# Kernel tuning notes

Hardware: AMD Instinct MI355X
Metric: run time of the kernel (lower is better)

Reference implementation:

```python
import jax, jax.numpy as jnp
import numpy as np

M, N, IN_DIM, NITER = 32, 32, 1024, 100
ALPHA, SIGMA = 0.3, 16.0  # sigma default = max(m, n) / 2
BATCH = 16384


def setup_inputs() -> dict:
    key = jax.random.key(0)
    k1, k2 = jax.random.split(key)
    x = jax.random.normal(k1, (BATCH, IN_DIM), dtype=jnp.float32)
    weights = jax.random.normal(k2, (IN_DIM, M * N), dtype=jnp.float32)
    ii, jj = jnp.meshgrid(jnp.arange(M), jnp.arange(N), indexing='ij')
    locations = jnp.stack([ii.ravel(), jj.ravel()], axis=1).astype(jnp.int32)  # (m*n, 2), row-major like the generator
    return {"x": x, "weights": weights, "locations": locations, "current_iter": 10}


def reference(x, weights, locations, current_iter):
    # x: (B, in_dim); weights: (in_dim, m*n); locations: (m*n, 2)
    B = x.shape[0]
    # Euclidean distances from each sample to each neuron, via ||a-b||^2 expansion
    x2 = jnp.sum(x * x, axis=1, keepdims=True)            # (B, 1)
    w2 = jnp.sum(weights * weights, axis=0)[None, :]      # (1, m*n)
    d2 = jnp.clip(x2 + w2 - 2.0 * (x @ weights), 0.0, None)
    dists = jnp.sqrt(d2)                                  # (B, m*n)
    loss_per = jnp.min(dists, axis=1)                     # (B,)
    bmu_index = jnp.argmin(dists, axis=1)                 # (B,)
    iter_correction = 1.0 - current_iter / NITER
    lr = ALPHA * iter_correction
    sigma = SIGMA * iter_correction
    loc_f = locations.astype(jnp.float32)                 # (m*n, 2)
    bmu_loc = loc_f[bmu_index]                            # (B, 2)
    # squared grid distance of every neuron to each sample's BMU
    dsq = jnp.sum((loc_f[None, :, :] - bmu_loc[:, None, :]) ** 2, axis=2)  # (B, m*n)
    lr_locations = jnp.exp(-dsq / (sigma * sigma)) * lr   # (B, m*n)
    # delta[i,k] = (1/B) * sum_b lr_locations[b,k] * (x[b,i] - weights[i,k])
    # computed without materializing the (B, in_dim, m*n) broadcast tensor
    pos = jnp.einsum('bk,bi->ik', lr_locations, x)        # (in_dim, m*n)
    neg = weights * jnp.sum(lr_locations, axis=0)[None, :]
    delta = (pos - neg) / B
    new_weights = weights + delta
    loss = jnp.sum(loss_per) / B
    return loss, new_weights
```

## Files before the change

### kernel.cpp

```cpp
#include <hip/hip_runtime.h>

typedef unsigned short u16;
typedef short bf16x8 __attribute__((ext_vector_type(8)));
typedef float f32x4 __attribute__((ext_vector_type(4)));

#define BATCH   16384
#define INDIM   1024
#define KNEUR   1024

__device__ __forceinline__ u16 f2bf(float f) {
  union { float f; unsigned u; } v; v.f = f;
  unsigned r = v.u + 0x7FFFu + ((v.u >> 16) & 1u);
  return (u16)(r >> 16);
}
__device__ __forceinline__ float bf2f(u16 h) {
  union { unsigned u; float f; } v; v.u = ((unsigned)h) << 16; return v.f;
}

#define GLDS(gp, lp) __builtin_amdgcn_global_load_lds( \
  (const __attribute__((address_space(1))) void*)(gp), \
  (__attribute__((address_space(3))) void*)(lp), 16, 0, 0)

#define RAWBAR() __builtin_amdgcn_s_barrier()
#define LGKM0() do { asm volatile("s_waitcnt lgkmcnt(0)" ::: "memory"); \
                     __builtin_amdgcn_sched_barrier(0); } while (0)
#define VMC6() asm volatile("s_waitcnt vmcnt(6)" ::: "memory")
#define VMC0() asm volatile("s_waitcnt vmcnt(0)" ::: "memory")

__global__ __launch_bounds__(256)
void k_prep(const float* __restrict__ x, u16* __restrict__ xb, float* __restrict__ x2,
            const float* __restrict__ w, u16* __restrict__ wt, float* __restrict__ w2,
            const int* __restrict__ loc, const int* __restrict__ itp,
            u16* __restrict__ Tb, float* __restrict__ Tf,
            float* __restrict__ Xf, int* __restrict__ cntcur, float* __restrict__ S) {
  __shared__ float tile[64][65];
  __shared__ float red[4][64];
  int bid = blockIdx.x;
  int t = threadIdx.x;
  if (bid < 4096) {
    int row = bid * 4 + (t >> 6);
    int l = t & 63;
    const float* xr = x + (size_t)row * INDIM;
    u16* xbr = xb + (size_t)row * INDIM;
    float s = 0.f;
    #pragma unroll
    for (int seg = 0; seg < 4; ++seg) {
      float4 v = *(const float4*)(xr + seg * 256 + l * 4);
      ushort4 o; o.x = f2bf(v.x); o.y = f2bf(v.y); o.z = f2bf(v.z); o.w = f2bf(v.w);
      *(ushort4*)(xbr + seg * 256 + l * 4) = o;
      s += v.x * v.x + v.y * v.y + v.z * v.z + v.w * v.w;
    }
    for (int m = 32; m; m >>= 1) s += __shfl_xor(s, m, 64);
    if (l == 0) x2[row] = s;
  } else if (bid < 8192) {
    int id = (bid - 4096) * 256 + t;
    int c = id >> 10, k = id & 1023;
    float corr = 1.f - (float)itp[0] / 100.f;
    float lr = 0.3f * corr;
    float sig = 16.f * corr;
    float inv_s2 = 1.f / (sig * sig);
    int di = loc[2 * c] - loc[2 * k];
    int dj = loc[2 * c + 1] - loc[2 * k + 1];
    float v = lr * __expf(-(float)(di * di + dj * dj) * inv_s2);
    Tf[id] = v;
    Tb[id] = f2bf(v);
    Xf[id] = 0.f;
    if (id < 2304) cntcur[id] = 0;
    if (id < 1024) S[id] = 0.f;
  } else if (bid < 8448) {
    int bb = bid - 8192;
    int bi = bb & 15;
    int bj = bb >> 4;
    int tx = t & 63, ty = t >> 6;
    int i0 = bj * 64, k0 = bi * 64;
    for (int r = ty; r < 64; r += 4)
      tile[r][tx] = w[(size_t)(i0 + r) * KNEUR + k0 + tx];
    __syncthreads();
    for (int r = ty; r < 64; r += 4)
      wt[(size_t)(k0 + r) * INDIM + i0 + tx] = f2bf(tile[tx][r]);
  } else {
    int tx = t & 63, ty = t >> 6;
    int k = (bid - 8448) * 64 + tx;
    float s = 0.f;
    for (int i = ty * 256; i < ty * 256 + 256; ++i) {
      float v = w[(size_t)i * KNEUR + k];
      s += v * v;
    }
    red[ty][tx] = s;
    __syncthreads();
    if (ty == 0) w2[k] = red[0][tx] + red[1][tx] + red[2][tx] + red[3][tx];
  }
}

__global__ __launch_bounds__(512, 2)
void k_gemm1_8p(const u16* __restrict__ A, const u16* __restrict__ Bm,
                const float* __restrict__ x2, const float* __restrict__ w2,
                float* __restrict__ pmin, int* __restrict__ pidx) {
  __shared__ __align__(16) u16 lds[2][2][2][128 * 64];
  __shared__ float s_rv[2][256];
  __shared__ int   s_ri[2][256];

  int bid = blockIdx.x;
  int swz = (bid & 7) * 32 + (bid >> 3);
  int mb = swz >> 2, nb = swz & 3;
  int tid = threadIdx.x;
  int lane = tid & 63;
  int wm = (tid >> 6) >> 1, wn = (tid >> 6) & 1;

  const size_t rowA0 = (size_t)mb * 256;
  const size_t rowB0 = (size_t)nb * 256;

  auto STAGE = [&](int u, int op, int qh) {
    if (u >= 16) return;
    const u16* src = (op == 0) ? (A + (rowA0 + qh * 128) * 1024)
                               : (Bm + (rowB0 + qh * 128) * 1024);
    int k0 = u * 64;
    u16* dst0 = &lds[u & 1][op][qh][0];
    #pragma unroll
    for (int j = 0; j < 2; ++j) {
      int s = j * 512 + tid;
      int r = s >> 3;
      int cs = (s & 7) ^ (r & 7);
      GLDS(src + (size_t)r * 1024 + k0 + cs * 8, dst0 + (size_t)s * 8);
    }
  };
  auto LDA = [&](bf16x8 (&a)[2][2], int db, int qm) {
    #pragma unroll
    for (int mt = 0; mt < 2; ++mt)
      #pragma unroll
      for (int kk = 0; kk < 2; ++kk) {
        int row = wm * 32 + mt * 16 + (lane & 15);
        int ch = (kk * 4 + (lane >> 4)) ^ (row & 7);
        a[mt][kk] = *(const bf16x8*)(&lds[db][0][qm][row * 64 + ch * 8]);
      }
  };
  auto LDB = [&](bf16x8 (&b)[4][2], int db, int qn) {
    #pragma unroll
    for (int nt = 0; nt < 4; ++nt)
      #pragma unroll
      for (int kk = 0; kk < 2; ++kk) {
        int row = wn * 64 + nt * 16 + (lane & 15);
        int ch = (kk * 4 + (lane >> 4)) ^ (row & 7);
        b[nt][kk] = *(const bf16x8*)(&lds[db][1][qn][row * 64 + ch * 8]);
      }
  };

  f32x4 acc[2][2][2][4];
  #pragma unroll
  for (int i = 0; i < 2; ++i)
    #pragma unroll
    for (int j = 0; j < 2; ++j)
      #pragma unroll
      for (int m = 0; m < 2; ++m)
        #pragma unroll
        for (int n = 0; n < 4; ++n) {
          acc[i][j][m][n][0] = 0.f; acc[i][j][m][n][1] = 0.f;
          acc[i][j][m][n][2] = 0.f; acc[i][j][m][n][3] = 0.f;
        }

  bf16x8 a[2][2], b0[4][2], b1[4][2];

  #define PHASE(accq, av, bv) do { \
    __builtin_amdgcn_s_setprio(1); \
    _Pragma("unroll") \
    for (int mt = 0; mt < 2; ++mt) \
      _Pragma("unroll") \
      for (int nt = 0; nt < 4; ++nt) \
        _Pragma("unroll") \
        for (int kk = 0; kk < 2; ++kk) \
          accq[mt][nt] = __builtin_amdgcn_mfma_f32_16x16x32_bf16(av[mt][kk], bv[nt][kk], accq[mt][nt], 0, 0, 0); \
    __builtin_amdgcn_s_setprio(0); \
  } while (0)

  STAGE(0, 0, 0); STAGE(0, 1, 1); STAGE(0, 0, 1); STAGE(0, 1, 0);
  STAGE(1, 0, 0); STAGE(1, 1, 1); STAGE(1, 0, 1);
  VMC6();
  RAWBAR();

  #pragma unroll 2
  for (int t = 0; t < 16; ++t) {
    int db = t & 1;
    LDA(a, db, 0); LDB(b0, db, 0);
    STAGE(t + 1, 1, 0);
    RAWBAR(); LGKM0();
    PHASE(acc[0][0], a, b0);
    RAWBAR();
    LDB(b1, db, 1);
    STAGE(t + 2, 0, 0);
    RAWBAR(); LGKM0();
    PHASE(acc[0][1], a, b1);
    RAWBAR();
    LDA(a, db, 1);
    STAGE(t + 2, 1, 1);
    RAWBAR(); LGKM0();
    PHASE(acc[1][1], a, b1);
    RAWBAR();
    STAGE(t + 2, 0, 1);
    RAWBAR(); LGKM0();
    PHASE(acc[1][0], a, b0);
    if (t < 14) { VMC6(); } else { VMC0(); }
    RAWBAR();
  }

  int g = lane >> 4, li = lane & 15;
  #pragma unroll
  for (int qm = 0; qm < 2; ++qm)
    #pragma unroll
    for (int mt = 0; mt < 2; ++mt)
      #pragma unroll
      for (int rr = 0; rr < 4; ++rr) {
        int lrow = qm * 128 + wm * 32 + mt * 16 + g * 4 + rr;
        float xv = x2[rowA0 + lrow];
        float v = 1e30f; int vi = 0x7fffffff;
        #pragma unroll
        for (int qn = 0; qn < 2; ++qn)
          #pragma unroll
          for (int nt = 0; nt < 4; ++nt) {
            int col = (int)rowB0 + qn * 128 + wn * 64 + nt * 16 + li;
            float d2 = xv + w2[col] - 2.f * acc[qm][qn][mt][nt][rr];
            if (d2 < v) { v = d2; vi = col; }
          }
        #pragma unroll
        for (int m = 1; m < 16; m <<= 1) {
          float ov = __shfl_xor(v, m, 64);
          int oi = __shfl_xor(vi, m, 64);
          if (ov < v || (ov == v && oi < vi)) { v = ov; vi = oi; }
        }
        if (li == 0) { s_rv[wn][lrow] = v; s_ri[wn][lrow] = vi; }
      }
  __syncthreads();
  if (tid < 256) {
    float v0 = s_rv[0][tid], v1 = s_rv[1][tid];
    int i0 = s_ri[0][tid], i1 = s_ri[1][tid];
    float v = v0; int vi = i0;
    if (v1 < v0 || (v1 == v0 && i1 < i0)) { v = v1; vi = i1; }
    size_t brow = rowA0 + tid;
    pmin[brow * 4 + nb] = v;
    pidx[brow * 4 + nb] = vi;
  }
  #undef PHASE
}

__global__ __launch_bounds__(256, 4)
void k_gemm2(const u16* __restrict__ A, const u16* __restrict__ Bm,
             float* __restrict__ outw) {
  __shared__ __align__(16) u16 ldsA[128 * 64];
  __shared__ __align__(16) u16 ldsB[128 * 64];

  int bid = blockIdx.x;
  int ks = bid & 3;
  int tile = bid >> 2;
  int mb = tile >> 3, nb = tile & 7;
  int ktlo = ks * 4, kthi = ktlo + 4;
  int lane = threadIdx.x & 63;
  int wid = threadIdx.x >> 6;
  int wr = wid >> 1, wc = wid & 1;

  f32x4 acc[4][4];
  #pragma unroll
  for (int i = 0; i < 4; ++i)
    #pragma unroll
    for (int j = 0; j < 4; ++j) { acc[i][j][0] = 0.f; acc[i][j][1] = 0.f; acc[i][j][2] = 0.f; acc[i][j][3] = 0.f; }

  const size_t rowA0 = (size_t)mb * 128;
  const size_t rowB0 = (size_t)nb * 128;

  for (int kt = ktlo; kt < kthi; ++kt) {
    int k0 = kt * 64;
    __syncthreads();
    #pragma unroll
    for (int q = 0; q < 4; ++q) {
      int p = q * 256 + wid * 64 + lane;
      int row = p >> 3;
      int clog = (p & 7) ^ (row & 7);
      GLDS(A + (rowA0 + row) * 1024 + k0 + clog * 8,
           ldsA + (size_t)(q * 256 + wid * 64) * 8);
    }
    #pragma unroll
    for (int q = 0; q < 4; ++q) {
      int p = q * 256 + wid * 64 + lane;
      int row = p >> 3;
      int clog = (p & 7) ^ (row & 7);
      GLDS(Bm + (rowB0 + row) * 1024 + k0 + clog * 8,
           ldsB + (size_t)(q * 256 + wid * 64) * 8);
    }
    __syncthreads();
    #pragma unroll
    for (int kk = 0; kk < 2; ++kk) {
      bf16x8 af[4], bfr[4];
      #pragma unroll
      for (int mt = 0; mt < 4; ++mt) {
        int row = wr * 64 + mt * 16 + (lane & 15);
        int ch = (kk * 4 + (lane >> 4)) ^ (row & 7);
        af[mt] = *(const bf16x8*)(ldsA + row * 64 + ch * 8);
      }
      #pragma unroll
      for (int nt = 0; nt < 4; ++nt) {
        int row = wc * 64 + nt * 16 + (lane & 15);
        int ch = (kk * 4 + (lane >> 4)) ^ (row & 7);
        bfr[nt] = *(const bf16x8*)(ldsB + row * 64 + ch * 8);
      }
      #pragma unroll
      for (int mt = 0; mt < 4; ++mt)
        #pragma unroll
        for (int nt = 0; nt < 4; ++nt)
          acc[mt][nt] = __builtin_amdgcn_mfma_f32_16x16x32_bf16(af[mt], bfr[nt], acc[mt][nt], 0, 0, 0);
    }
  }

  const float invB = 1.f / (float)BATCH;
  #pragma unroll
  for (int mt = 0; mt < 4; ++mt)
    #pragma unroll
    for (int nt = 0; nt < 4; ++nt)
      #pragma unroll
      for (int r = 0; r < 4; ++r) {
        int i = (int)rowA0 + wr * 64 + mt * 16 + (lane >> 4) * 4 + r;
        int k = (int)rowB0 + wc * 64 + nt * 16 + (lane & 15);
        atomicAdd(&outw[(size_t)i * KNEUR + k], acc[mt][nt][r] * invB);
      }
}

__global__ void k_bmu_scan(const float* __restrict__ pmin, const int* __restrict__ pidx,
                           int* __restrict__ bmu, float* __restrict__ lpart,
                           int* __restrict__ cnt, int* __restrict__ ticket,
                           int* __restrict__ cursor, float* __restrict__ cntf,
                           float* __restrict__ out) {
  int t = threadIdx.x;
  int b = blockIdx.x * 256 + t;
  float v = 1e30f; int vi = 0;
  #pragma unroll
  for (int j = 0; j < 4; ++j) {
    float pv = pmin[(size_t)b * 4 + j];
    if (pv < v) { v = pv; vi = pidx[(size_t)b * 4 + j]; }
  }
  bmu[b] = vi;
  atomicAdd(&cnt[vi], 1);
  float d = sqrtf(fmaxf(v, 0.f));
  __shared__ float red[256];
  red[t] = d;
  __syncthreads();
  for (int s = 128; s > 0; s >>= 1) {
    if (t < s) red[t] += red[t + s];
    __syncthreads();
  }
  if (t == 0) lpart[blockIdx.x] = red[0];

  __threadfence();
  __shared__ int is_last;
  if (t == 0) is_last = (atomicAdd(ticket, 1) == 63);
  __syncthreads();
  if (!is_last) return;

  __shared__ int sc[256];
  int4 c4 = *(const int4*)(cnt + 4 * t);
  int tsum = c4.x + c4.y + c4.z + c4.w;
  sc[t] = tsum;
  __syncthreads();
  for (int off = 1; off < 256; off <<= 1) {
    int val = sc[t];
    int add = (t >= off) ? sc[t - off] : 0;
    __syncthreads();
    sc[t] = val + add;
    __syncthreads();
  }
  int excl = sc[t] - tsum;
  cursor[4 * t + 0] = excl;
  cursor[4 * t + 1] = excl + c4.x;
  cursor[4 * t + 2] = excl + c4.x + c4.y;
  cursor[4 * t + 3] = excl + c4.x + c4.y + c4.z;
  cntf[4 * t + 0] = (float)c4.x;
  cntf[4 * t + 1] = (float)c4.y;
  cntf[4 * t + 2] = (float)c4.z;
  cntf[4 * t + 3] = (float)c4.w;
  if (t < 64) {
    float l = lpart[t];
    for (int m = 32; m; m >>= 1) l += __shfl_xor(l, m, 64);
    if (t == 0) out[0] = l * (1.f / (float)BATCH);
  }
}

__global__ void k_place_S(const int* __restrict__ bmu, int* __restrict__ cursor,
                          int* __restrict__ perm,
                          const float* __restrict__ cntf, const float* __restrict__ Tf,
                          float* __restrict__ S) {
  int bid = blockIdx.x;
  int t = threadIdx.x;
  if (bid < 64) {
    int b = bid * 256 + t;
    int c = bmu[b];
    int p = atomicAdd(&cursor[c], 1);
    perm[p] = b;
  } else {
    int chunk = bid - 64;
    int cchunk = chunk >> 2;
    int kb = chunk & 3;
    int k = kb * 256 + t;
    float s = 0.f;
    for (int c = cchunk * 64; c < cchunk * 64 + 64; ++c)
      s += cntf[c] * Tf[(size_t)c * KNEUR + k];
    atomicAdd(&S[k], s);
  }
}

__global__ __launch_bounds__(256)
void k_xsum2(const int* __restrict__ perm, const int* __restrict__ bmu,
             const u16* __restrict__ xb, float* __restrict__ Xf) {
  int t = threadIdx.x;
  int m0 = blockIdx.x * 32;
  int pm[32], cl[32];
  #pragma unroll
  for (int j = 0; j < 32; ++j) pm[j] = perm[m0 + j];
  #pragma unroll
  for (int j = 0; j < 32; ++j) cl[j] = bmu[pm[j]];
  float a0 = 0.f, a1 = 0.f, a2 = 0.f, a3 = 0.f;
  int ccur = cl[0];
  #pragma unroll
  for (int j = 0; j < 32; ++j) {
    if (cl[j] != ccur) {
      float* p = Xf + (size_t)ccur * INDIM + 4 * t;
      atomicAdd(p + 0, a0); atomicAdd(p + 1, a1);
      atomicAdd(p + 2, a2); atomicAdd(p + 3, a3);
      a0 = a1 = a2 = a3 = 0.f;
      ccur = cl[j];
    }
    ushort4 v = *(const ushort4*)(xb + (size_t)pm[j] * INDIM + t * 4);
    a0 += bf2f(v.x); a1 += bf2f(v.y); a2 += bf2f(v.z); a3 += bf2f(v.w);
  }
  float* p = Xf + (size_t)ccur * INDIM + 4 * t;
  atomicAdd(p + 0, a0); atomicAdd(p + 1, a1);
  atomicAdd(p + 2, a2); atomicAdd(p + 3, a3);
}

__global__ void k_trans_base(const float* __restrict__ Xf, u16* __restrict__ xst,
                             const float* __restrict__ w, const float* __restrict__ S,
                             float* __restrict__ outw) {
  int bid = blockIdx.x;
  int t = threadIdx.x;
  if (bid < 256) {
    __shared__ float tile[64][65];
    int bc = bid & 15;
    int bi = bid >> 4;
    int tx = t & 63, ty = t >> 6;
    int c0 = bc * 64, i0 = bi * 64;
    for (int r = ty; r < 64; r += 4)
      tile[r][tx] = Xf[(size_t)(c0 + r) * INDIM + i0 + tx];
    __syncthreads();
    for (int r = ty; r < 64; r += 4)
      xst[(size_t)(i0 + r) * KNEUR + c0 + tx] = f2bf(tile[tx][r]);
  } else {
    const float invB = 1.f / (float)BATCH;
    size_t base = ((size_t)(bid - 256) * 256 + t) * 16;
    int k = (int)(base & 1023);
    #pragma unroll
    for (int seg = 0; seg < 4; ++seg) {
      float4 wv = *(const float4*)(w + base + seg * 4);
      float4 sv = *(const float4*)(S + k + seg * 4);
      outw[base + seg * 4 + 0] = wv.x - wv.x * sv.x * invB;
      outw[base + seg * 4 + 1] = wv.y - wv.y * sv.y * invB;
      outw[base + seg * 4 + 2] = wv.z - wv.z * sv.z * invB;
      outw[base + seg * 4 + 3] = wv.w - wv.w * sv.w * invB;
    }
  }
}

extern "C" void kernel_launch(void* const* d_in, const int* in_sizes, int n_in,
                              void* d_out, int out_size, void* d_ws, size_t ws_size,
                              hipStream_t stream) {
  const float* x = (const float*)d_in[0];
  const float* w = (const float*)d_in[1];
  const int* loc = (const int*)d_in[2];
  const int* it = (const int*)d_in[3];
  float* out = (float*)d_out;

  char* ws = (char*)d_ws;
  size_t off = 0;
  auto alloc = [&](size_t bytes) -> void* {
    void* p = ws + off;
    off += (bytes + 255) & ~(size_t)255;
    return p;
  };
  u16* xb    = (u16*)  alloc((size_t)BATCH * INDIM * 2);
  u16* wt    = (u16*)  alloc((size_t)KNEUR * INDIM * 2);
  u16* Tb    = (u16*)  alloc((size_t)KNEUR * KNEUR * 2);
  float* Tf  = (float*)alloc((size_t)KNEUR * KNEUR * 4);
  u16* xst   = (u16*)  alloc((size_t)INDIM * KNEUR * 2);
  float* x2  = (float*)alloc((size_t)BATCH * 4);
  float* w2  = (float*)alloc((size_t)KNEUR * 4);
  float* pmin= (float*)alloc((size_t)BATCH * 4 * 4);
  int* pidx  = (int*)  alloc((size_t)BATCH * 4 * 4);
  int* bmu   = (int*)  alloc((size_t)BATCH * 4);
  float* cntf= (float*)alloc((size_t)KNEUR * 4);
  float* S   = (float*)alloc((size_t)KNEUR * 4);
  float* lpart=(float*)alloc(64 * 4);
  float* Xf  = (float*)alloc((size_t)KNEUR * INDIM * 4);
  int* cntcur= (int*)  alloc((size_t)2304 * 4);
  int* perm  = (int*)  alloc((size_t)BATCH * 4);
  if (off > ws_size) return;

  int* cnt = cntcur;
  int* cursor = cntcur + KNEUR;
  int* ticket = cntcur + 2 * KNEUR;
  float* outw = out + 1;

  k_prep<<<8464, 256, 0, stream>>>(x, xb, x2, w, wt, w2, loc, it, Tb, Tf, Xf, cntcur, S);
  k_gemm1_8p<<<256, 512, 0, stream>>>(xb, wt, x2, w2, pmin, pidx);
  k_bmu_scan<<<64, 256, 0, stream>>>(pmin, pidx, bmu, lpart, cnt, ticket, cursor, cntf, out);
  k_place_S<<<128, 256, 0, stream>>>(bmu, cursor, perm, cntf, Tf, S);
  k_xsum2<<<BATCH / 32, 256, 0, stream>>>(perm, bmu, xb, Xf);
  k_trans_base<<<512, 256, 0, stream>>>(Xf, xst, w, S, outw);
  k_gemm2<<<256, 256, 0, stream>>>(xst, Tb, outw);
}
```

Measured before the change: 155.8 us.

## Replace gemm2 atomic split-K with 8-way partial buffers and reduction kernel

The second GEMM now splits K eight ways (512 blocks) and writes each split's partial tile with plain stores into a scratch buffer that reuses the bf16 x workspace. A new k_wupd kernel sums the eight partials and applies the weight-base update in one pass, so the old fused transpose/base kernel keeps only the transpose. This removes a million float atomics and the read-modify-write ordering against the base init, at the cost of one extra launch and about 32 MB of partial-buffer traffic. Separately, gemm1's main loop drops its unroll-2 pragma and gains an lgkmcnt(8) wait before the barrier.

```diff
diff --git a/kernel.cpp b/kernel.cpp
--- a/kernel.cpp
+++ b/kernel.cpp
@@ -24,6 +24,7 @@
 #define RAWBAR() __builtin_amdgcn_s_barrier()
 #define LGKM0() do { asm volatile("s_waitcnt lgkmcnt(0)" ::: "memory"); \
                      __builtin_amdgcn_sched_barrier(0); } while (0)
+#define LGKM8() asm volatile("s_waitcnt lgkmcnt(8)" ::: "memory")
 #define VMC6() asm volatile("s_waitcnt vmcnt(6)" ::: "memory")
 #define VMC0() asm volatile("s_waitcnt vmcnt(0)" ::: "memory")
 
@@ -177,11 +178,11 @@
   VMC6();
   RAWBAR();
 
-  #pragma unroll 2
   for (int t = 0; t < 16; ++t) {
     int db = t & 1;
     LDA(a, db, 0); LDB(b0, db, 0);
     STAGE(t + 1, 1, 0);
+    LGKM8();
     RAWBAR(); LGKM0();
     PHASE(acc[0][0], a, b0);
     RAWBAR();
@@ -243,15 +244,15 @@
 
 __global__ __launch_bounds__(256, 4)
 void k_gemm2(const u16* __restrict__ A, const u16* __restrict__ Bm,
-             float* __restrict__ outw) {
+             float* __restrict__ P8) {
   __shared__ __align__(16) u16 ldsA[128 * 64];
   __shared__ __align__(16) u16 ldsB[128 * 64];
 
   int bid = blockIdx.x;
-  int ks = bid & 3;
-  int tile = bid >> 2;
+  int ks = bid & 7;
+  int tile = bid >> 3;
   int mb = tile >> 3, nb = tile & 7;
-  int ktlo = ks * 4, kthi = ktlo + 4;
+  int ktlo = ks * 2, kthi = ktlo + 2;
   int lane = threadIdx.x & 63;
   int wid = threadIdx.x >> 6;
   int wr = wid >> 1, wc = wid & 1;
@@ -308,7 +309,7 @@
     }
   }
 
-  const float invB = 1.f / (float)BATCH;
+  float* base = P8 + ((size_t)ks << 20);
   #pragma unroll
   for (int mt = 0; mt < 4; ++mt)
     #pragma unroll
@@ -317,7 +318,7 @@
       for (int r = 0; r < 4; ++r) {
         int i = (int)rowA0 + wr * 64 + mt * 16 + (lane >> 4) * 4 + r;
         int k = (int)rowB0 + wc * 64 + nt * 16 + (lane & 15);
-        atomicAdd(&outw[(size_t)i * KNEUR + k], acc[mt][nt][r] * invB);
+        base[(size_t)i * KNEUR + k] = acc[mt][nt][r];
       }
 }
 
@@ -432,36 +433,39 @@
   atomicAdd(p + 2, a2); atomicAdd(p + 3, a3);
 }
 
-__global__ void k_trans_base(const float* __restrict__ Xf, u16* __restrict__ xst,
-                             const float* __restrict__ w, const float* __restrict__ S,
-                             float* __restrict__ outw) {
+__global__ void k_trans(const float* __restrict__ Xf, u16* __restrict__ xst) {
   int bid = blockIdx.x;
   int t = threadIdx.x;
-  if (bid < 256) {
-    __shared__ float tile[64][65];
-    int bc = bid & 15;
-    int bi = bid >> 4;
-    int tx = t & 63, ty = t >> 6;
-    int c0 = bc * 64, i0 = bi * 64;
-    for (int r = ty; r < 64; r += 4)
-      tile[r][tx] = Xf[(size_t)(c0 + r) * INDIM + i0 + tx];
-    __syncthreads();
-    for (int r = ty; r < 64; r += 4)
-      xst[(size_t)(i0 + r) * KNEUR + c0 + tx] = f2bf(tile[tx][r]);
-  } else {
-    const float invB = 1.f / (float)BATCH;
-    size_t base = ((size_t)(bid - 256) * 256 + t) * 16;
-    int k = (int)(base & 1023);
-    #pragma unroll
-    for (int seg = 0; seg < 4; ++seg) {
-      float4 wv = *(const float4*)(w + base + seg * 4);
-      float4 sv = *(const float4*)(S + k + seg * 4);
-      outw[base + seg * 4 + 0] = wv.x - wv.x * sv.x * invB;
-      outw[base + seg * 4 + 1] = wv.y - wv.y * sv.y * invB;
-      outw[base + seg * 4 + 2] = wv.z - wv.z * sv.z * invB;
-      outw[base + seg * 4 + 3] = wv.w - wv.w * sv.w * invB;
-    }
-  }
+  __shared__ float tile[64][65];
+  int bc = bid & 15;
+  int bi = bid >> 4;
+  int tx = t & 63, ty = t >> 6;
+  int c0 = bc * 64, i0 = bi * 64;
+  for (int r = ty; r < 64; r += 4)
+    tile[r][tx] = Xf[(size_t)(c0 + r) * INDIM + i0 + tx];
+  __syncthreads();
+  for (int r = ty; r < 64; r += 4)
+    xst[(size_t)(i0 + r) * KNEUR + c0 + tx] = f2bf(tile[tx][r]);
+}
+
+__global__ void k_wupd(const float* __restrict__ P8, const float* __restrict__ w,
+                       const float* __restrict__ S, float* __restrict__ outw) {
+  const float invB = 1.f / (float)BATCH;
+  int id4 = blockIdx.x * 256 + threadIdx.x;
+  size_t base = (size_t)id4 * 4;
+  int k = (int)(base & 1023);
+  float4 s0 = *(const float4*)(P8 + base);
+  #pragma unroll
+  for (int j = 1; j < 8; ++j) {
+    float4 pj = *(const float4*)(P8 + ((size_t)j << 20) + base);
+    s0.x += pj.x; s0.y += pj.y; s0.z += pj.z; s0.w += pj.w;
+  }
+  float4 wv = *(const float4*)(w + base);
+  float4 sv = *(const float4*)(S + k);
+  outw[base + 0] = wv.x + (s0.x - wv.x * sv.x) * invB;
+  outw[base + 1] = wv.y + (s0.y - wv.y * sv.y) * invB;
+  outw[base + 2] = wv.z + (s0.z - wv.z * sv.z) * invB;
+  outw[base + 3] = wv.w + (s0.w - wv.w * sv.w) * invB;
 }
 
 extern "C" void kernel_launch(void* const* d_in, const int* in_sizes, int n_in,
@@ -502,12 +506,14 @@
   int* cursor = cntcur + KNEUR;
   int* ticket = cntcur + 2 * KNEUR;
   float* outw = out + 1;
+  float* P8 = (float*)xb;
 
   k_prep<<<8464, 256, 0, stream>>>(x, xb, x2, w, wt, w2, loc, it, Tb, Tf, Xf, cntcur, S);
   k_gemm1_8p<<<256, 512, 0, stream>>>(xb, wt, x2, w2, pmin, pidx);
   k_bmu_scan<<<64, 256, 0, stream>>>(pmin, pidx, bmu, lpart, cnt, ticket, cursor, cntf, out);
   k_place_S<<<128, 256, 0, stream>>>(bmu, cursor, perm, cntf, Tf, S);
   k_xsum2<<<BATCH / 32, 256, 0, stream>>>(perm, bmu, xb, Xf);
-  k_trans_base<<<512, 256, 0, stream>>>(Xf, xst, w, S, outw);
-  k_gemm2<<<256, 256, 0, stream>>>(xst, Tb, outw);
-}
+  k_trans<<<256, 256, 0, stream>>>(Xf, xst);
+  k_gemm2<<<512, 256, 0, stream>>>(xst, Tb, P8);
+  k_wupd<<<1024, 256, 0, stream>>>(P8, w, S, outw);
+}
```

After: 144.7 us. 7.1% less time.

## Fuse weight-base epilogue into second GEMM, drop split-K atomics, double-buffer LDS

Applied to the files above, without the earlier changes.

The second GEMM changes from split-K with 128x128 tiles and float atomicAdd into an output pre-initialised by the transpose kernel to full-K 64x64 tiles. It double-buffers the LDS stages and writes w + (acc - w*S)/B directly in its epilogue. This removes the separate base-weight pass and the atomic read-modify-write traffic, at the cost of smaller tiles and a 16-step serial K loop per block. The first GEMM also drops its unroll-2 pragma and adds an lgkmcnt(8) wait before a barrier.

```diff
diff --git a/kernel.cpp b/kernel.cpp
--- a/kernel.cpp
+++ b/kernel.cpp
@@ -24,6 +24,7 @@
 #define RAWBAR() __builtin_amdgcn_s_barrier()
 #define LGKM0() do { asm volatile("s_waitcnt lgkmcnt(0)" ::: "memory"); \
                      __builtin_amdgcn_sched_barrier(0); } while (0)
+#define LGKM8() asm volatile("s_waitcnt lgkmcnt(8)" ::: "memory")
 #define VMC6() asm volatile("s_waitcnt vmcnt(6)" ::: "memory")
 #define VMC0() asm volatile("s_waitcnt vmcnt(0)" ::: "memory")
 
@@ -177,11 +178,11 @@
   VMC6();
   RAWBAR();
 
-  #pragma unroll 2
   for (int t = 0; t < 16; ++t) {
     int db = t & 1;
     LDA(a, db, 0); LDB(b0, db, 0);
     STAGE(t + 1, 1, 0);
+    LGKM8();
     RAWBAR(); LGKM0();
     PHASE(acc[0][0], a, b0);
     RAWBAR();
@@ -241,83 +242,89 @@
   #undef PHASE
 }
 
-__global__ __launch_bounds__(256, 4)
-void k_gemm2(const u16* __restrict__ A, const u16* __restrict__ Bm,
-             float* __restrict__ outw) {
-  __shared__ __align__(16) u16 ldsA[128 * 64];
-  __shared__ __align__(16) u16 ldsB[128 * 64];
+__global__ __launch_bounds__(256, 2)
+void k_gemm2f(const u16* __restrict__ A, const u16* __restrict__ Bm,
+              const float* __restrict__ w, const float* __restrict__ S,
+              float* __restrict__ outw) {
+  __shared__ __align__(16) u16 ldsA[2][64 * 64];
+  __shared__ __align__(16) u16 ldsB[2][64 * 64];
 
   int bid = blockIdx.x;
-  int ks = bid & 3;
-  int tile = bid >> 2;
-  int mb = tile >> 3, nb = tile & 7;
-  int ktlo = ks * 4, kthi = ktlo + 4;
-  int lane = threadIdx.x & 63;
-  int wid = threadIdx.x >> 6;
+  int mb = bid >> 4, nb = bid & 15;
+  int tid = threadIdx.x;
+  int lane = tid & 63;
+  int wid = tid >> 6;
   int wr = wid >> 1, wc = wid & 1;
 
-  f32x4 acc[4][4];
-  #pragma unroll
-  for (int i = 0; i < 4; ++i)
-    #pragma unroll
-    for (int j = 0; j < 4; ++j) { acc[i][j][0] = 0.f; acc[i][j][1] = 0.f; acc[i][j][2] = 0.f; acc[i][j][3] = 0.f; }
-
-  const size_t rowA0 = (size_t)mb * 128;
-  const size_t rowB0 = (size_t)nb * 128;
-
-  for (int kt = ktlo; kt < kthi; ++kt) {
-    int k0 = kt * 64;
-    __syncthreads();
-    #pragma unroll
-    for (int q = 0; q < 4; ++q) {
-      int p = q * 256 + wid * 64 + lane;
-      int row = p >> 3;
-      int clog = (p & 7) ^ (row & 7);
-      GLDS(A + (rowA0 + row) * 1024 + k0 + clog * 8,
-           ldsA + (size_t)(q * 256 + wid * 64) * 8);
+  const size_t rowA0 = (size_t)mb * 64;
+  const size_t rowB0 = (size_t)nb * 64;
+
+  auto STAGE2 = [&](int u, int buf) {
+    int k0 = u * 64;
+    #pragma unroll
+    for (int j = 0; j < 2; ++j) {
+      int s = j * 256 + tid;
+      int r = s >> 3;
+      int cs = (s & 7) ^ (r & 7);
+      GLDS(A + (rowA0 + r) * 1024 + k0 + cs * 8, &ldsA[buf][s * 8]);
+      GLDS(Bm + (rowB0 + r) * 1024 + k0 + cs * 8, &ldsB[buf][s * 8]);
     }
-    #pragma unroll
-    for (int q = 0; q < 4; ++q) {
-      int p = q * 256 + wid * 64 + lane;
-      int row = p >> 3;
-      int clog = (p & 7) ^ (row & 7);
-      GLDS(Bm + (rowB0 + row) * 1024 + k0 + clog * 8,
-           ldsB + (size_t)(q * 256 + wid * 64) * 8);
-    }
-    __syncthreads();
-    #pragma unroll
-    for (int kk = 0; kk < 2; ++kk) {
-      bf16x8 af[4], bfr[4];
-      #pragma unroll
-      for (int mt = 0; mt < 4; ++mt) {
-        int row = wr * 64 + mt * 16 + (lane & 15);
+  };
+
+  f32x4 acc[2][2];
+  #pragma unroll
+  for (int i = 0; i < 2; ++i)
+    #pragma unroll
+    for (int j = 0; j < 2; ++j) { acc[i][j][0] = 0.f; acc[i][j][1] = 0.f; acc[i][j][2] = 0.f; acc[i][j][3] = 0.f; }
+
+  STAGE2(0, 0);
+  VMC0();
+  RAWBAR();
+
+  for (int t = 0; t < 16; ++t) {
+    int buf = t & 1;
+    if (t < 15) STAGE2(t + 1, buf ^ 1);
+    bf16x8 af[2][2], bfr[2][2];
+    #pragma unroll
+    for (int mt = 0; mt < 2; ++mt)
+      #pragma unroll
+      for (int kk = 0; kk < 2; ++kk) {
+        int row = wr * 32 + mt * 16 + (lane & 15);
         int ch = (kk * 4 + (lane >> 4)) ^ (row & 7);
-        af[mt] = *(const bf16x8*)(ldsA + row * 64 + ch * 8);
+        af[mt][kk] = *(const bf16x8*)(&ldsA[buf][row * 64 + ch * 8]);
       }
-      #pragma unroll
-      for (int nt = 0; nt < 4; ++nt) {
-        int row = wc * 64 + nt * 16 + (lane & 15);
+    #pragma unroll
+    for (int nt = 0; nt < 2; ++nt)
+      #pragma unroll
+      for (int kk = 0; kk < 2; ++kk) {
+        int row = wc * 32 + nt * 16 + (lane & 15);
         int ch = (kk * 4 + (lane >> 4)) ^ (row & 7);
-        bfr[nt] = *(const bf16x8*)(ldsB + row * 64 + ch * 8);
+        bfr[nt][kk] = *(const bf16x8*)(&ldsB[buf][row * 64 + ch * 8]);
       }
-      #pragma unroll
-      for (int mt = 0; mt < 4; ++mt)
+    LGKM0();
+    __builtin_amdgcn_s_setprio(1);
+    #pragma unroll
+    for (int mt = 0; mt < 2; ++mt)
+      #pragma unroll
+      for (int nt = 0; nt < 2; ++nt)
         #pragma unroll
-        for (int nt = 0; nt < 4; ++nt)
-          acc[mt][nt] = __builtin_amdgcn_mfma_f32_16x16x32_bf16(af[mt], bfr[nt], acc[mt][nt], 0, 0, 0);
-    }
+        for (int kk = 0; kk < 2; ++kk)
+          acc[mt][nt] = __builtin_amdgcn_mfma_f32_16x16x32_bf16(af[mt][kk], bfr[nt][kk], acc[mt][nt], 0, 0, 0);
+    __builtin_amdgcn_s_setprio(0);
+    if (t < 15) { VMC0(); RAWBAR(); }
   }
 
   const float invB = 1.f / (float)BATCH;
   #pragma unroll
-  for (int mt = 0; mt < 4; ++mt)
-    #pragma unroll
-    for (int nt = 0; nt < 4; ++nt)
+  for (int mt = 0; mt < 2; ++mt)
+    #pragma unroll
+    for (int nt = 0; nt < 2; ++nt)
       #pragma unroll
       for (int r = 0; r < 4; ++r) {
-        int i = (int)rowA0 + wr * 64 + mt * 16 + (lane >> 4) * 4 + r;
-        int k = (int)rowB0 + wc * 64 + nt * 16 + (lane & 15);
-        atomicAdd(&outw[(size_t)i * KNEUR + k], acc[mt][nt][r] * invB);
+        int i = (int)rowA0 + wr * 32 + mt * 16 + (lane >> 4) * 4 + r;
+        int k = (int)rowB0 + wc * 32 + nt * 16 + (lane & 15);
+        float wv = w[(size_t)i * KNEUR + k];
+        outw[(size_t)i * KNEUR + k] = wv + (acc[mt][nt][r] - wv * S[k]) * invB;
       }
 }
 
@@ -432,36 +439,19 @@
   atomicAdd(p + 2, a2); atomicAdd(p + 3, a3);
 }
 
-__global__ void k_trans_base(const float* __restrict__ Xf, u16* __restrict__ xst,
-                             const float* __restrict__ w, const float* __restrict__ S,
-                             float* __restrict__ outw) {
+__global__ void k_trans(const float* __restrict__ Xf, u16* __restrict__ xst) {
   int bid = blockIdx.x;
   int t = threadIdx.x;
-  if (bid < 256) {
-    __shared__ float tile[64][65];
-    int bc = bid & 15;
-    int bi = bid >> 4;
-    int tx = t & 63, ty = t >> 6;
-    int c0 = bc * 64, i0 = bi * 64;
-    for (int r = ty; r < 64; r += 4)
-      tile[r][tx] = Xf[(size_t)(c0 + r) * INDIM + i0 + tx];
-    __syncthreads();
-    for (int r = ty; r < 64; r += 4)
-      xst[(size_t)(i0 + r) * KNEUR + c0 + tx] = f2bf(tile[tx][r]);
-  } else {
-    const float invB = 1.f / (float)BATCH;
-    size_t base = ((size_t)(bid - 256) * 256 + t) * 16;
-    int k = (int)(base & 1023);
-    #pragma unroll
-    for (int seg = 0; seg < 4; ++seg) {
-      float4 wv = *(const float4*)(w + base + seg * 4);
-      float4 sv = *(const float4*)(S + k + seg * 4);
-      outw[base + seg * 4 + 0] = wv.x - wv.x * sv.x * invB;
-      outw[base + seg * 4 + 1] = wv.y - wv.y * sv.y * invB;
-      outw[base + seg * 4 + 2] = wv.z - wv.z * sv.z * invB;
-      outw[base + seg * 4 + 3] = wv.w - wv.w * sv.w * invB;
-    }
-  }
+  __shared__ float tile[64][65];
+  int bc = bid & 15;
+  int bi = bid >> 4;
+  int tx = t & 63, ty = t >> 6;
+  int c0 = bc * 64, i0 = bi * 64;
+  for (int r = ty; r < 64; r += 4)
+    tile[r][tx] = Xf[(size_t)(c0 + r) * INDIM + i0 + tx];
+  __syncthreads();
+  for (int r = ty; r < 64; r += 4)
+    xst[(size_t)(i0 + r) * KNEUR + c0 + tx] = f2bf(tile[tx][r]);
 }
 
 extern "C" void kernel_launch(void* const* d_in, const int* in_sizes, int n_in,
@@ -508,6 +498,6 @@
   k_bmu_scan<<<64, 256, 0, stream>>>(pmin, pidx, bmu, lpart, cnt, ticket, cursor, cntf, out);
   k_place_S<<<128, 256, 0, stream>>>(bmu, cursor, perm, cntf, Tf, S);
   k_xsum2<<<BATCH / 32, 256, 0, stream>>>(perm, bmu, xb, Xf);
-  k_trans_base<<<512, 256, 0, stream>>>(Xf, xst, w, S, outw);
-  k_gemm2<<<256, 256, 0, stream>>>(xst, Tb, outw);
-}
+  k_trans<<<256, 256, 0, stream>>>(Xf, xst);
+  k_gemm2f<<<256, 256, 0, stream>>>(xst, Tb, w, S, outw);
+}
```

Measured after the change: 135.1 us (median of 3 runs). 1.15x faster.
